# Kernel optimization log

Hardware: AMD Instinct MI355X
Metric: run time of the kernel (lower is better)

## Reference

```python
import jax, jax.numpy as jnp
import numpy as np

WS = 4      # window_size (RSUT5 default)
SHIFT = 2   # window_size // 2
NH = 8      # num_heads
DIM = 256
H0 = W0 = T0 = 32
B0 = 1


def _ln(x, g, b, eps=1e-5):
    m = x.mean(-1, keepdims=True)
    v = ((x - m) ** 2).mean(-1, keepdims=True)
    return (x - m) / jnp.sqrt(v + eps) * g + b


def _rel_index(ws):
    c = np.stack(np.meshgrid(np.arange(ws), np.arange(ws), np.arange(ws), indexing='ij')).reshape(3, -1)
    r = (c[:, :, None] - c[:, None, :]).transpose(1, 2, 0) + (ws - 1)
    return jnp.asarray((r[..., 0] * (2 * ws - 1) + r[..., 1]) * (2 * ws - 1) + r[..., 2])


def _partition(x, ws):
    B, H, W, T, C = x.shape
    x = x.reshape(B, H // ws, ws, W // ws, ws, T // ws, ws, C)
    return x.transpose(0, 1, 3, 5, 2, 4, 6, 7).reshape(-1, ws ** 3, C)


def _reverse(w, ws, B, H, W, T):
    C = w.shape[-1]
    x = w.reshape(B, H // ws, W // ws, T // ws, ws, ws, ws, C)
    return x.transpose(0, 1, 4, 2, 5, 3, 6, 7).reshape(B, H, W, T, C)


def _attn_mask(H, W, T, ws, ss):
    # static (numpy) replica of Block.createmask; H,W,T divisible by ws here
    img = np.zeros((H, W, T), np.float32)
    sls = (slice(0, -ws), slice(-ws, -ss), slice(-ss, None))
    cnt = 0
    for h in sls:
        for w in sls:
            for t in sls:
                img[h, w, t] = cnt
                cnt += 1
    mw = img.reshape(H // ws, ws, W // ws, ws, T // ws, ws).transpose(0, 2, 4, 1, 3, 5).reshape(-1, ws ** 3)
    d = mw[:, None, :] - mw[:, :, None]
    return jnp.asarray(np.where(d != 0, -100.0, 0.0).astype(np.float32))


def _swin(x, H, W, T, shift, mask, n1g, n1b, qkvw, qkvb, rpb, projw, projb, n2g, n2b, fc1w, fc1b, fc2w, fc2b):
    B, L, C = x.shape
    N = WS ** 3
    hd = C // NH
    shortcut = x
    x = _ln(x, n1g, n1b).reshape(B, H, W, T, C)
    if shift:
        x = jnp.roll(x, (-shift, -shift, -shift), axis=(1, 2, 3))
    xw = _partition(x, WS)                                        # [B*nW, N, C]
    qkv = (xw @ qkvw.T + qkvb).reshape(-1, N, 3, NH, hd).transpose(2, 0, 3, 1, 4)
    q, k, v = qkv[0], qkv[1], qkv[2]                              # [B*nW, NH, N, hd]
    attn = jnp.einsum('bhnd,bhmd->bhnm', q * (hd ** -0.5), k)
    attn = attn + rpb[_rel_index(WS)].transpose(2, 0, 1)[None]    # relative position bias
    if mask is not None:
        nW = mask.shape[0]
        attn = (attn.reshape(B, nW, NH, N, N) + mask[None, :, None]).reshape(-1, NH, N, N)
    attn = jax.nn.softmax(attn, axis=-1)
    out = jnp.einsum('bhnm,bhmd->bhnd', attn, v).transpose(0, 2, 1, 3).reshape(-1, N, C)
    out = out @ projw.T + projb
    x = _reverse(out, WS, B, H, W, T)
    if shift:
        x = jnp.roll(x, (shift, shift, shift), axis=(1, 2, 3))
    x = shortcut + x.reshape(B, L, C)
    h = _ln(x, n2g, n2b)
    h = jax.nn.gelu(h @ fc1w.T + fc1b, approximate=False) @ fc2w.T + fc2b
    return x + h


def setup_inputs() -> dict:
    key = jax.random.key(0)
    ks = iter(jax.random.split(key, 16))
    def rn(shape, s=0.02):
        return jax.random.normal(next(ks), shape, jnp.float32) * s
    d = {'x': jax.random.normal(next(ks), (B0, H0 * W0 * T0, DIM), jnp.float32),
         'H': H0, 'W': W0, 'T': T0,
         'norm_g': jnp.ones((DIM,), jnp.float32), 'norm_b': jnp.zeros((DIM,), jnp.float32)}
    for p in ('w', 's'):
        d[p + 'n1g'] = jnp.ones((DIM,), jnp.float32); d[p + 'n1b'] = jnp.zeros((DIM,), jnp.float32)
        d[p + 'qkvw'] = rn((3 * DIM, DIM)); d[p + 'qkvb'] = jnp.zeros((3 * DIM,), jnp.float32)
        d[p + 'rpb'] = rn(((2 * WS - 1) ** 3, NH))
        d[p + 'projw'] = rn((DIM, DIM)); d[p + 'projb'] = jnp.zeros((DIM,), jnp.float32)
        d[p + 'n2g'] = jnp.ones((DIM,), jnp.float32); d[p + 'n2b'] = jnp.zeros((DIM,), jnp.float32)
        d[p + 'fc1w'] = rn((4 * DIM, DIM)); d[p + 'fc1b'] = jnp.zeros((4 * DIM,), jnp.float32)
        d[p + 'fc2w'] = rn((DIM, 4 * DIM)); d[p + 'fc2b'] = jnp.zeros((DIM,), jnp.float32)
    return d


def reference(x, H, W, T, norm_g, norm_b,
              wn1g, wn1b, wqkvw, wqkvb, wrpb, wprojw, wprojb, wn2g, wn2b, wfc1w, wfc1b, wfc2w, wfc2b,
              sn1g, sn1b, sqkvw, sqkvb, srpb, sprojw, sprojb, sn2g, sn2b, sfc1w, sfc1b, sfc2w, sfc2b):
    mask = _attn_mask(H, W, T, WS, SHIFT)
    x = _swin(x, H, W, T, 0, None, wn1g, wn1b, wqkvw, wqkvb, wrpb, wprojw, wprojb, wn2g, wn2b, wfc1w, wfc1b, wfc2w, wfc2b)
    x = _swin(x, H, W, T, SHIFT, mask, sn1g, sn1b, sqkvw, sqkvb, srpb, sprojw, sprojb, sn2g, sn2b, sfc1w, sfc1b, sfc2w, sfc2b)
    B, L, C = x.shape
    # Block.norm + toConv: [B, L, C] -> [B, C, H, W, T]
    return _ln(x, norm_g, norm_b).reshape(B, H, W, T, C).transpose(0, 4, 1, 2, 3)
```

## Files before the change

### kernel.cpp

```cpp
#include <hip/hip_runtime.h>

typedef unsigned short u16;
typedef unsigned int   u32;
typedef __bf16 bfx8 __attribute__((ext_vector_type(8)));
typedef float  fx4  __attribute__((ext_vector_type(4)));

__device__ __forceinline__ u16 f2b(float f) {
    union { float f; u32 i; } v; v.f = f;
    u32 r = (v.i + 0x7fffu + ((v.i >> 16) & 1u)) >> 16;
    return (u16)r;
}
__device__ __forceinline__ u32 pk(float a, float b) {
    return (u32)f2b(a) | ((u32)f2b(b) << 16);
}
__device__ __forceinline__ float gelu(float x) {
    float u = 0.7978845608028654f * x * (1.0f + 0.044715f * x * x);
    float e = __expf(2.0f * u);
    float t = 1.0f - 2.0f / (e + 1.0f);
    return 0.5f * x * (1.0f + t);
}

__device__ __forceinline__ void gl2lds16(const u16* g, u16* l) {
    __builtin_amdgcn_global_load_lds(
        (const __attribute__((address_space(1))) u32*)(const void*)g,
        (__attribute__((address_space(3))) u32*)(void*)l, 16, 0, 0);
}

__device__ __forceinline__ int map_token(int r, int shift) {
    int win = r >> 6, n = r & 63;
    int wh = win >> 6, ww = (win >> 3) & 7, wt = win & 7;
    int h = wh * 4 + (n >> 4);
    int w = ww * 4 + ((n >> 2) & 3);
    int t = wt * 4 + (n & 3);
    h = (h + shift) & 31; w = (w + shift) & 31; t = (t + shift) & 31;
    return (h << 10) | (w << 5) | t;
}

struct CvtArgs { const float* src[8]; int cum[9]; };
__global__ __launch_bounds__(256) void cvt_kernel(CvtArgs a, u16* __restrict__ dst) {
    int g = (blockIdx.x * 256 + threadIdx.x) * 4;
    int t = 0;
    #pragma unroll
    for (int i = 1; i < 8; i++) t += (g >= a.cum[i]);
    int local = g - a.cum[t];
    float4 f = *(const float4*)(a.src[t] + local);
    uint2 o; o.x = pk(f.x, f.y); o.y = pk(f.z, f.w);
    *(uint2*)(dst + g) = o;
}

__global__ __launch_bounds__(64) void bias_kernel(const float* __restrict__ rpbW, const float* __restrict__ rpbS,
                                                  float* __restrict__ tab) {
    int bx = blockIdx.x;
    int shifted = bx >= 8;
    int idx = shifted ? bx - 8 : bx;
    int cls = shifted ? (idx >> 3) : 0;
    int head = idx & 7;
    const float* rpb = shifted ? rpbS : rpbW;
    float* out = tab + (size_t)bx * 4096;
    int i = threadIdx.x;
    int ih = i >> 4, iw = (i >> 2) & 3, it = i & 3;
    int mh = (cls >> 2) & 1, mw = (cls >> 1) & 1, mt = cls & 1;
    int labn = (mh ? (1 + (ih >> 1)) : 0) * 9 + (mw ? (1 + (iw >> 1)) : 0) * 3 + (mt ? (1 + (it >> 1)) : 0);
    for (int j = 0; j < 64; j++) {
        int jh = j >> 4, jw = (j >> 2) & 3, jt = j & 3;
        float v = rpb[(((ih - jh + 3) * 7 + (iw - jw + 3)) * 7 + (it - jt + 3)) * 8 + head];
        int labm = (mh ? (1 + (jh >> 1)) : 0) * 9 + (mw ? (1 + (jw >> 1)) : 0) * 3 + (mt ? (1 + (jt >> 1)) : 0);
        if (labm != labn) v -= 100.0f;
        out[i * 64 + j] = v;
    }
}

template<int GATHER, int F32OUT>
__global__ __launch_bounds__(256) void ln_kernel(const float* __restrict__ resid,
                                                 const float* __restrict__ g, const float* __restrict__ b,
                                                 void* __restrict__ outp, int shift) {
    int lane = threadIdx.x & 63;
    int row  = blockIdx.x * 4 + (threadIdx.x >> 6);
    int src  = GATHER ? map_token(row, shift) : row;
    float4 x = ((const float4*)(resid + src * 256))[lane];
    float s1 = x.x + x.y + x.z + x.w;
    float s2 = x.x * x.x + x.y * x.y + x.z * x.z + x.w * x.w;
    #pragma unroll
    for (int off = 1; off < 64; off <<= 1) { s1 += __shfl_xor(s1, off); s2 += __shfl_xor(s2, off); }
    float mean = s1 * (1.0f / 256.0f);
    float var  = s2 * (1.0f / 256.0f) - mean * mean;
    float rstd = rsqrtf(var + 1e-5f);
    int c = lane * 4;
    float4 gv = *(const float4*)(g + c);
    float4 bv = *(const float4*)(b + c);
    float y0 = (x.x - mean) * rstd * gv.x + bv.x;
    float y1 = (x.y - mean) * rstd * gv.y + bv.y;
    float y2 = (x.z - mean) * rstd * gv.z + bv.z;
    float y3 = (x.w - mean) * rstd * gv.w + bv.w;
    if (F32OUT) {
        float4 o; o.x = y0; o.y = y1; o.z = y2; o.w = y3;
        *(float4*)((float*)outp + row * 256 + c) = o;
    } else {
        uint2 o; o.x = pk(y0, y1); o.y = pk(y2, y3);
        *(uint2*)((u16*)outp + row * 256 + c) = o;
    }
}

template<int EPI>
__global__ __launch_bounds__(256) void gemm5(const u16* __restrict__ A, const u16* __restrict__ W,
                                             const float* __restrict__ bias,
                                             u16* __restrict__ outb, float* __restrict__ resid,
                                             const float* __restrict__ xin,
                                             int Nout, int K, int shift) {
    __shared__ u16 As[128 * 32];
    __shared__ u16 Bs[128 * 32];
    int tid = threadIdx.x;
    int lane = tid & 63, w = tid >> 6;
    int wm = w >> 1, wn = w & 1;
    int m0 = blockIdx.x * 128, n0 = blockIdx.y * 128;
    int lr = lane & 15, q = lane >> 4;
    int sw = q ^ ((lr >> 1) & 3);

    int s0 = tid, s1 = 256 + tid;
    int r0 = s0 >> 2, r1 = s1 >> 2;
    int k0 = (s0 & 3) ^ ((r0 >> 1) & 3);
    int k1 = (s1 & 3) ^ ((r1 >> 1) & 3);
    const u16* ga0 = A + (size_t)(m0 + r0) * K + k0 * 8;
    const u16* ga1 = A + (size_t)(m0 + r1) * K + k1 * 8;
    const u16* gb0 = W + (size_t)(n0 + r0) * K + k0 * 8;
    const u16* gb1 = W + (size_t)(n0 + r1) * K + k1 * 8;
    u16* la0 = As + s0 * 8; u16* la1 = As + s1 * 8;
    u16* lb0 = Bs + s0 * 8; u16* lb1 = Bs + s1 * 8;

    const u16* rdA = As + (wm * 64 + lr) * 32 + sw * 8;
    const u16* rdB = Bs + (wn * 64 + lr) * 32 + sw * 8;

    fx4 acc[4][4] = {};

    for (int kt = 0; kt < K; kt += 32) {
        __syncthreads();
        gl2lds16(ga0, la0); gl2lds16(ga1, la1);
        gl2lds16(gb0, lb0); gl2lds16(gb1, lb1);
        ga0 += 32; ga1 += 32; gb0 += 32; gb1 += 32;
        __syncthreads();
        bfx8 af[4], bfr[4];
        #pragma unroll
        for (int t = 0; t < 4; t++) {
            af[t]  = *(const bfx8*)(rdA + t * 512);
            bfr[t] = *(const bfx8*)(rdB + t * 512);
        }
        #pragma unroll
        for (int i = 0; i < 4; i++)
            #pragma unroll
            for (int j = 0; j < 4; j++)
                acc[i][j] = __builtin_amdgcn_mfma_f32_16x16x32_bf16(bfr[j], af[i], acc[i][j], 0, 0, 0);
    }

    float4 bv[4];
    #pragma unroll
    for (int j = 0; j < 4; j++) bv[j] = *(const float4*)(bias + n0 + wn * 64 + j * 16 + q * 4);
    #pragma unroll
    for (int i = 0; i < 4; i++) {
        int gr = m0 + wm * 64 + i * 16 + lr;
        int orow = (EPI >= 3) ? map_token(gr, shift) : gr;
        #pragma unroll
        for (int j = 0; j < 4; j++) {
            int gc = n0 + wn * 64 + j * 16 + q * 4;
            float v0 = acc[i][j][0] + bv[j].x;
            float v1 = acc[i][j][1] + bv[j].y;
            float v2 = acc[i][j][2] + bv[j].z;
            float v3 = acc[i][j][3] + bv[j].w;
            if (EPI == 0) {
                uint2 o; o.x = pk(v0, v1); o.y = pk(v2, v3);
                *(uint2*)(outb + (size_t)gr * Nout + gc) = o;
            } else if (EPI == 1) {
                uint2 o; o.x = pk(gelu(v0), gelu(v1)); o.y = pk(gelu(v2), gelu(v3));
                *(uint2*)(outb + (size_t)gr * Nout + gc) = o;
            } else if (EPI == 4) {
                float4 xv = *(const float4*)(xin + orow * 256 + gc);
                float4 rv;
                rv.x = xv.x + v0; rv.y = xv.y + v1; rv.z = xv.z + v2; rv.w = xv.w + v3;
                *(float4*)(resid + orow * 256 + gc) = rv;
            } else {
                float4 rv = *(float4*)(resid + orow * 256 + gc);
                rv.x += v0; rv.y += v1; rv.z += v2; rv.w += v3;
                *(float4*)(resid + orow * 256 + gc) = rv;
            }
        }
    }
}

__global__ __launch_bounds__(128) void attn3(const u16* __restrict__ qkv, const float* __restrict__ tab,
                                             u16* __restrict__ outb, int masked) {
    __shared__ u16 Pl[2][64][72];
    __shared__ u16 VT[2][32][72];
    int w = threadIdx.x >> 6, lane = threadIdx.x & 63;
    int id = blockIdx.x * 2 + w;
    int win = id >> 3, head = id & 7;
    int lr = lane & 15, q = lane >> 4;
    const u16* base = qkv + (size_t)win * 64 * 768 + head * 32;

    bfx8 qf[4], kf[4];
    #pragma unroll
    for (int t = 0; t < 4; t++) {
        const u16* rq = base + (lr + 16 * t) * 768 + q * 8;
        qf[t] = *(const bfx8*)(rq);
        kf[t] = *(const bfx8*)(rq + 256);
    }
    {
        const u16* rv = base + lane * 768 + 512;
        #pragma unroll
        for (int c = 0; c < 32; c += 8) {
            bfx8 vv = *(const bfx8*)(rv + c);
            #pragma unroll
            for (int j = 0; j < 8; j++) VT[w][c + j][lane] = ((const u16*)&vv)[j];
        }
    }

    fx4 sT[4][4] = {};
    #pragma unroll
    for (int jt = 0; jt < 4; jt++)
        #pragma unroll
        for (int it = 0; it < 4; it++)
            sT[jt][it] = __builtin_amdgcn_mfma_f32_16x16x32_bf16(kf[jt], qf[it], sT[jt][it], 0, 0, 0);

    int wh = win >> 6, ww = (win >> 3) & 7, wt = win & 7;
    int slab = masked ? (8 + ((((wh == 7) ? 4 : 0) | ((ww == 7) ? 2 : 0) | ((wt == 7) ? 1 : 0)) * 8) + head)
                      : head;
    const float* bt = tab + (size_t)slab * 4096 + q * 4;
    const float scale = 0.17677669529663687f;

    #pragma unroll
    for (int it = 0; it < 4; it++) {
        int i = lr + 16 * it;
        const float* br = bt + i * 64;
        float sv[4][4];
        float mx = -1e30f;
        #pragma unroll
        for (int jt = 0; jt < 4; jt++) {
            float4 bb = *(const float4*)(br + 16 * jt);
            sv[jt][0] = sT[jt][it][0] * scale + bb.x;
            sv[jt][1] = sT[jt][it][1] * scale + bb.y;
            sv[jt][2] = sT[jt][it][2] * scale + bb.z;
            sv[jt][3] = sT[jt][it][3] * scale + bb.w;
            mx = fmaxf(mx, fmaxf(fmaxf(sv[jt][0], sv[jt][1]), fmaxf(sv[jt][2], sv[jt][3])));
        }
        mx = fmaxf(mx, __shfl_xor(mx, 16));
        mx = fmaxf(mx, __shfl_xor(mx, 32));
        float sum = 0.f;
        #pragma unroll
        for (int jt = 0; jt < 4; jt++)
            #pragma unroll
            for (int r = 0; r < 4; r++) { sv[jt][r] = __expf(sv[jt][r] - mx); sum += sv[jt][r]; }
        sum += __shfl_xor(sum, 16);
        sum += __shfl_xor(sum, 32);
        float inv = 1.0f / sum;
        #pragma unroll
        for (int jt = 0; jt < 4; jt++) {
            uint2 pw;
            pw.x = pk(sv[jt][0] * inv, sv[jt][1] * inv);
            pw.y = pk(sv[jt][2] * inv, sv[jt][3] * inv);
            *(uint2*)&Pl[w][i][q * 4 + 16 * jt] = pw;
        }
    }

    fx4 o[4][2] = {};
    #pragma unroll
    for (int kk = 0; kk < 2; kk++) {
        bfx8 pf[4], vf[2];
        #pragma unroll
        for (int it = 0; it < 4; it++) pf[it] = *(const bfx8*)&Pl[w][lr + 16 * it][q * 8 + 32 * kk];
        #pragma unroll
        for (int dt = 0; dt < 2; dt++) vf[dt] = *(const bfx8*)&VT[w][lr + 16 * dt][q * 8 + 32 * kk];
        #pragma unroll
        for (int it = 0; it < 4; it++)
            #pragma unroll
            for (int dt = 0; dt < 2; dt++)
                o[it][dt] = __builtin_amdgcn_mfma_f32_16x16x32_bf16(vf[dt], pf[it], o[it][dt], 0, 0, 0);
    }

    u16* ob = outb + (size_t)win * 64 * 256 + head * 32;
    #pragma unroll
    for (int it = 0; it < 4; it++) {
        int i = lr + 16 * it;
        #pragma unroll
        for (int dt = 0; dt < 2; dt++) {
            uint2 ov;
            ov.x = pk(o[it][dt][0], o[it][dt][1]);
            ov.y = pk(o[it][dt][2], o[it][dt][3]);
            *(uint2*)(ob + i * 256 + dt * 16 + q * 4) = ov;
        }
    }
}

__global__ __launch_bounds__(256) void transpose_f32(const float* __restrict__ in, float* __restrict__ out) {
    __shared__ float tile[64][65];
    int t0 = blockIdx.x * 64;
    int c0 = blockIdx.y * 64;
    int row = threadIdx.x >> 2, cg = (threadIdx.x & 3) * 16;
    const float* src = in + (t0 + row) * 256 + c0 + cg;
    #pragma unroll
    for (int j = 0; j < 16; j += 4) {
        float4 v = *(const float4*)(src + j);
        tile[row][cg + j] = v.x; tile[row][cg + j + 1] = v.y;
        tile[row][cg + j + 2] = v.z; tile[row][cg + j + 3] = v.w;
    }
    __syncthreads();
    float tmp[16];
    #pragma unroll
    for (int j = 0; j < 16; j++) tmp[j] = tile[cg + j][row];
    float* dst = out + (c0 + row) * 32768 + t0 + cg;
    #pragma unroll
    for (int j = 0; j < 4; j++) *(float4*)(dst + 4 * j) = *(float4*)(tmp + 4 * j);
}

extern "C" void kernel_launch(void* const* d_in, const int* in_sizes, int n_in,
                              void* d_out, int out_size, void* d_ws, size_t ws_size,
                              hipStream_t stream) {
    const float* x      = (const float*)d_in[0];
    const float* norm_g = (const float*)d_in[4];
    const float* norm_b = (const float*)d_in[5];

    char* wsb = (char*)d_ws;
    float* resid = (float*)wsb;
    u16*   xn    = (u16*)(wsb + (size_t)32 * 1024 * 1024);
    u16*   big   = (u16*)(wsb + (size_t)48 * 1024 * 1024);
    u16*   attnb = (u16*)(wsb + (size_t)96 * 1024 * 1024);
    u16*   wb    = (u16*)(wsb + (size_t)112 * 1024 * 1024);
    float* tab   = (float*)(wsb + (size_t)115 * 1024 * 1024);
    float* xnf   = (float*)(wsb + (size_t)48 * 1024 * 1024);

    CvtArgs ca;
    static const int offs[9] = {0, 196608, 262144, 524288, 786432, 983040, 1048576, 1310720, 1572864};
    for (int i = 0; i < 9; i++) ca.cum[i] = offs[i];
    ca.src[0] = (const float*)d_in[6 + 2];
    ca.src[1] = (const float*)d_in[6 + 5];
    ca.src[2] = (const float*)d_in[6 + 9];
    ca.src[3] = (const float*)d_in[6 + 11];
    ca.src[4] = (const float*)d_in[19 + 2];
    ca.src[5] = (const float*)d_in[19 + 5];
    ca.src[6] = (const float*)d_in[19 + 9];
    ca.src[7] = (const float*)d_in[19 + 11];
    cvt_kernel<<<1536, 256, 0, stream>>>(ca, wb);
    bias_kernel<<<72, 64, 0, stream>>>((const float*)d_in[6 + 4], (const float*)d_in[19 + 4], tab);

    for (int blk = 0; blk < 2; blk++) {
        void* const* P = d_in + 6 + blk * 13;
        const float* n1g  = (const float*)P[0];
        const float* n1b  = (const float*)P[1];
        const float* qkvb = (const float*)P[3];
        const float* pjb  = (const float*)P[6];
        const float* n2g  = (const float*)P[7];
        const float* n2b  = (const float*)P[8];
        const float* f1b  = (const float*)P[10];
        const float* f2b_ = (const float*)P[12];
        const u16* qkvw = wb + offs[0] + blk * 786432;
        const u16* pjw  = wb + offs[1] + blk * 786432;
        const u16* f1w  = wb + offs[2] + blk * 786432;
        const u16* f2w  = wb + offs[3] + blk * 786432;
        int shift = blk ? 2 : 0;
        const float* ln1src = blk ? resid : x;

        ln_kernel<1, 0><<<8192, 256, 0, stream>>>(ln1src, n1g, n1b, xn, shift);
        gemm5<0><<<dim3(256, 6), 256, 0, stream>>>(xn, qkvw, qkvb, big, nullptr, nullptr, 768, 256, 0);
        attn3<<<2048, 128, 0, stream>>>(big, tab, attnb, blk);
        if (blk == 0)
            gemm5<4><<<dim3(256, 2), 256, 0, stream>>>(attnb, pjw, pjb, nullptr, resid, x, 256, 256, 0);
        else
            gemm5<3><<<dim3(256, 2), 256, 0, stream>>>(attnb, pjw, pjb, nullptr, resid, nullptr, 256, 256, shift);
        ln_kernel<0, 0><<<8192, 256, 0, stream>>>(resid, n2g, n2b, xn, 0);
        gemm5<1><<<dim3(256, 8), 256, 0, stream>>>(xn, f1w, f1b, big, nullptr, nullptr, 1024, 256, 0);
        gemm5<2><<<dim3(256, 2), 256, 0, stream>>>(big, f2w, f2b_, nullptr, resid, nullptr, 256, 1024, 0);
    }

    ln_kernel<0, 1><<<8192, 256, 0, stream>>>(resid, norm_g, norm_b, xnf, 0);
    transpose_f32<<<dim3(512, 4), 256, 0, stream>>>(xnf, (float*)d_out);
}
```

Before: 534.5 us.

## Stage full K=256 slabs in LDS per GEMM iteration with XOR swizzle

```diff
diff --git a/kernel.cpp b/kernel.cpp
--- a/kernel.cpp
+++ b/kernel.cpp
@@ -102,53 +102,50 @@
 }
 
 template<int EPI>
-__global__ __launch_bounds__(256) void gemm5(const u16* __restrict__ A, const u16* __restrict__ W,
+__global__ __launch_bounds__(256) void gemm6(const u16* __restrict__ A, const u16* __restrict__ W,
                                              const float* __restrict__ bias,
                                              u16* __restrict__ outb, float* __restrict__ resid,
                                              const float* __restrict__ xin,
                                              int Nout, int K, int shift) {
-    __shared__ u16 As[128 * 32];
-    __shared__ u16 Bs[128 * 32];
+    __shared__ u16 As[128 * 256];
+    __shared__ u16 Bs[128 * 256];
     int tid = threadIdx.x;
     int lane = tid & 63, w = tid >> 6;
     int wm = w >> 1, wn = w & 1;
     int m0 = blockIdx.x * 128, n0 = blockIdx.y * 128;
     int lr = lane & 15, q = lane >> 4;
-    int sw = q ^ ((lr >> 1) & 3);
-
-    int s0 = tid, s1 = 256 + tid;
-    int r0 = s0 >> 2, r1 = s1 >> 2;
-    int k0 = (s0 & 3) ^ ((r0 >> 1) & 3);
-    int k1 = (s1 & 3) ^ ((r1 >> 1) & 3);
-    const u16* ga0 = A + (size_t)(m0 + r0) * K + k0 * 8;
-    const u16* ga1 = A + (size_t)(m0 + r1) * K + k1 * 8;
-    const u16* gb0 = W + (size_t)(n0 + r0) * K + k0 * 8;
-    const u16* gb1 = W + (size_t)(n0 + r1) * K + k1 * 8;
-    u16* la0 = As + s0 * 8; u16* la1 = As + s1 * 8;
-    u16* lb0 = Bs + s0 * 8; u16* lb1 = Bs + s1 * 8;
-
-    const u16* rdA = As + (wm * 64 + lr) * 32 + sw * 8;
-    const u16* rdB = Bs + (wn * 64 + lr) * 32 + sw * 8;
+    int lr7 = lr & 7;
 
     fx4 acc[4][4] = {};
 
-    for (int kt = 0; kt < K; kt += 32) {
+    int srow = tid >> 5;
+    int sG0  = tid & 31;
+    for (int kt = 0; kt < K; kt += 256) {
         __syncthreads();
-        gl2lds16(ga0, la0); gl2lds16(ga1, la1);
-        gl2lds16(gb0, lb0); gl2lds16(gb1, lb1);
-        ga0 += 32; ga1 += 32; gb0 += 32; gb1 += 32;
+        #pragma unroll
+        for (int rd = 0; rd < 16; rd++) {
+            int row = rd * 8 + srow;
+            int G = sG0 ^ (row & 7);
+            int s = row * 32 + sG0;
+            gl2lds16(A + (size_t)(m0 + row) * K + kt + G * 8, As + s * 8);
+            gl2lds16(W + (size_t)(n0 + row) * K + kt + G * 8, Bs + s * 8);
+        }
         __syncthreads();
-        bfx8 af[4], bfr[4];
-        #pragma unroll
-        for (int t = 0; t < 4; t++) {
-            af[t]  = *(const bfx8*)(rdA + t * 512);
-            bfr[t] = *(const bfx8*)(rdB + t * 512);
-        }
-        #pragma unroll
-        for (int i = 0; i < 4; i++)
-            #pragma unroll
-            for (int j = 0; j < 4; j++)
-                acc[i][j] = __builtin_amdgcn_mfma_f32_16x16x32_bf16(bfr[j], af[i], acc[i][j], 0, 0, 0);
+        #pragma unroll
+        for (int ks = 0; ks < 8; ks++) {
+            int gg = (4 * ks + q) ^ lr7;
+            bfx8 af[4], bfr[4];
+            #pragma unroll
+            for (int t = 0; t < 4; t++) {
+                af[t]  = *(const bfx8*)(As + (wm * 64 + t * 16 + lr) * 256 + gg * 8);
+                bfr[t] = *(const bfx8*)(Bs + (wn * 64 + t * 16 + lr) * 256 + gg * 8);
+            }
+            #pragma unroll
+            for (int i = 0; i < 4; i++)
+                #pragma unroll
+                for (int j = 0; j < 4; j++)
+                    acc[i][j] = __builtin_amdgcn_mfma_f32_16x16x32_bf16(bfr[j], af[i], acc[i][j], 0, 0, 0);
+        }
     }
 
     float4 bv[4];
@@ -357,15 +354,15 @@
         const float* ln1src = blk ? resid : x;
 
         ln_kernel<1, 0><<<8192, 256, 0, stream>>>(ln1src, n1g, n1b, xn, shift);
-        gemm5<0><<<dim3(256, 6), 256, 0, stream>>>(xn, qkvw, qkvb, big, nullptr, nullptr, 768, 256, 0);
+        gemm6<0><<<dim3(256, 6), 256, 0, stream>>>(xn, qkvw, qkvb, big, nullptr, nullptr, 768, 256, 0);
         attn3<<<2048, 128, 0, stream>>>(big, tab, attnb, blk);
         if (blk == 0)
-            gemm5<4><<<dim3(256, 2), 256, 0, stream>>>(attnb, pjw, pjb, nullptr, resid, x, 256, 256, 0);
+            gemm6<4><<<dim3(256, 2), 256, 0, stream>>>(attnb, pjw, pjb, nullptr, resid, x, 256, 256, 0);
         else
-            gemm5<3><<<dim3(256, 2), 256, 0, stream>>>(attnb, pjw, pjb, nullptr, resid, nullptr, 256, 256, shift);
+            gemm6<3><<<dim3(256, 2), 256, 0, stream>>>(attnb, pjw, pjb, nullptr, resid, nullptr, 256, 256, shift);
         ln_kernel<0, 0><<<8192, 256, 0, stream>>>(resid, n2g, n2b, xn, 0);
-        gemm5<1><<<dim3(256, 8), 256, 0, stream>>>(xn, f1w, f1b, big, nullptr, nullptr, 1024, 256, 0);
-        gemm5<2><<<dim3(256, 2), 256, 0, stream>>>(big, f2w, f2b_, nullptr, resid, nullptr, 256, 1024, 0);
+        gemm6<1><<<dim3(256, 8), 256, 0, stream>>>(xn, f1w, f1b, big, nullptr, nullptr, 1024, 256, 0);
+        gemm6<2><<<dim3(256, 2), 256, 0, stream>>>(big, f2w, f2b_, nullptr, resid, nullptr, 256, 1024, 0);
     }
 
     ln_kernel<0, 1><<<8192, 256, 0, stream>>>(resid, norm_g, norm_b, xnf, 0);
```

After: 650.2 us. 21.6% more time.
